# Kernel optimization log

Hardware: AMD Instinct MI355X
Metric: run time of the kernel (lower is better)

## Reference

```python
import jax, jax.numpy as jnp
import numpy as np

N = 100000        # nodes
E = 1600000       # edges (N * avg_degree 16)
D_IN = 128
D_OUT = 32
OBS_T = 60        # observation_time -> decay table size 60*OBS_T = 3600
T_MAX = 60 * OBS_T


def setup_inputs() -> dict:
    key = jax.random.key(0)
    ks = jax.random.split(key, 8)
    inp = {
        "input": jax.random.normal(ks[0], (N, D_IN), dtype=jnp.float32),
        "W": jax.random.normal(ks[1], (D_IN, D_OUT), dtype=jnp.float32) * (np.sqrt(2.0) / np.sqrt(D_IN)),
        # decay weights are abs(normal(0, 0.02)) in the original; rand*0.04 is same scale
        "decay_weight1": jnp.abs(jax.random.normal(ks[2], (T_MAX, 1), dtype=jnp.float32) * 0.02),
        "decay_weight2": jnp.abs(jax.random.normal(ks[3], (T_MAX, 1), dtype=jnp.float32) * 0.02),
        "edge_row": jax.random.randint(ks[4], (E,), 0, N, dtype=jnp.int32),
        "edge_col": jax.random.randint(ks[5], (E,), 0, N, dtype=jnp.int32),
        # zero-based interval index; equals (adj_value - 1) of the original code
        "edge_time": jax.random.randint(ks[6], (E,), 0, T_MAX, dtype=jnp.int32),
        "arrive_time": jax.random.randint(ks[7], (N,), 0, T_MAX, dtype=jnp.int32),
        "observation_time": OBS_T,
    }
    return inp


def reference(input, W, decay_weight1, decay_weight2,
              edge_row, edge_col, edge_time, arrive_time, observation_time):
    n_nodes = input.shape[0]
    # h = relu(input @ W)  [N, D_OUT]
    h = jax.nn.relu(jnp.matmul(input, W))
    # one-hot(interval) @ decay_weight1 == embedding lookup  -> per-edge decay scalar
    decay = decay_weight1[edge_time, 0]                        # [E]
    # SpecialSpmm: out[i] = sum_{edges (i,j)} decay_e * h[j]  (gather-scale-scatter)
    msgs = decay[:, None] * h[edge_col]                        # [E, D_OUT]
    h_prime = jax.ops.segment_sum(msgs, edge_row, num_segments=n_nodes)
    # outlayer window decay: one-hot(60*T - arrive - 1) @ decay_weight2 == lookup
    win_idx = 60 * observation_time - arrive_time - 1          # [N] in [0, 60*T)
    h_prime = decay_weight2[win_idx, 0][:, None] * h_prime
    return h_prime
```

## Files before the change

### kernel.cpp

```cpp
#include <hip/hip_runtime.h>

#define N_NODES 100000
#define N_EDGES 1600000
#define D_IN    128
#define D_OUT   32
#define RPB     16
#define NB      (N_NODES / RPB)
#define CROWS   2048
#define NCB     49
#define FPC     (CROWS / RPB)
#define NSH     8
#define CAP_A   4500
#define DEPTH   48
#define CAPF    352
#define GRID_A  2048
#define EPB_A   ((N_EDGES + GRID_A - 1) / GRID_A)

typedef __attribute__((ext_vector_type(8))) short bf16x8;
typedef __attribute__((ext_vector_type(4))) float f32x4;

__device__ inline short f2bf(float f) {
    union { float f; unsigned u; } v; v.f = f;
    unsigned r = (v.u + 0x7FFFu + ((v.u >> 16) & 1u)) >> 16;
    return (short)r;
}
__device__ inline float bf2f(unsigned short b) {
    return __uint_as_float((unsigned)b << 16);
}

__global__ __launch_bounds__(256) void wconv_kernel(
    const float* __restrict__ W, short* __restrict__ WbT)
{
    const int i = blockIdx.x * 256 + threadIdx.x;
    if (i >= D_IN * D_OUT) return;
    const int k = i >> 5, c = i & 31;
    WbT[c * D_IN + k] = f2bf(W[i]);
}

__global__ __launch_bounds__(256) void gemm_mfma_kernel(
    const float* __restrict__ in, const short* __restrict__ WbT,
    unsigned short* __restrict__ h16)
{
    const int wave = threadIdx.x >> 6;
    const int lane = threadIdx.x & 63;
    const int r0   = blockIdx.x * 64 + wave * 16;
    const int c16  = lane & 15;
    const int quad = lane >> 4;

    int ra = r0 + c16;
    if (ra >= N_NODES) ra = N_NODES - 1;
    const float* arow = in + (size_t)ra * D_IN;

    f32x4 acc0 = {0.f, 0.f, 0.f, 0.f};
    f32x4 acc1 = {0.f, 0.f, 0.f, 0.f};

#pragma unroll
    for (int q = 0; q < 4; ++q) {
        const float* ap = arow + q * 32 + quad * 8;
        f32x4 a0 = *(const f32x4*)(ap);
        f32x4 a1 = *(const f32x4*)(ap + 4);
        bf16x8 af;
        af[0] = f2bf(a0.x); af[1] = f2bf(a0.y); af[2] = f2bf(a0.z); af[3] = f2bf(a0.w);
        af[4] = f2bf(a1.x); af[5] = f2bf(a1.y); af[6] = f2bf(a1.z); af[7] = f2bf(a1.w);
        bf16x8 b0 = *(const bf16x8*)(WbT + (c16)      * D_IN + q * 32 + quad * 8);
        bf16x8 b1 = *(const bf16x8*)(WbT + (c16 + 16) * D_IN + q * 32 + quad * 8);
        acc0 = __builtin_amdgcn_mfma_f32_16x16x32_bf16(af, b0, acc0, 0, 0, 0);
        acc1 = __builtin_amdgcn_mfma_f32_16x16x32_bf16(af, b1, acc1, 0, 0, 0);
    }

#pragma unroll
    for (int i = 0; i < 4; ++i) {
        const int rr = r0 + quad * 4 + i;
        if (rr < N_NODES) {
            h16[(size_t)rr * D_OUT + c16]      = (unsigned short)f2bf(fmaxf(acc0[i], 0.f));
            h16[(size_t)rr * D_OUT + c16 + 16] = (unsigned short)f2bf(fmaxf(acc1[i], 0.f));
        }
    }
}

__global__ __launch_bounds__(256) void phaseA_kernel(
    const int* __restrict__ erow, const int* __restrict__ ecol,
    const int* __restrict__ etime, const float* __restrict__ dw1,
    int* __restrict__ gcur,
    uint2* __restrict__ segA)
{
    __shared__ uint2 lbin[NCB][DEPTH];
    __shared__ int   lcnt[NCB];
    __shared__ int   gbase[NCB];

    const int tid   = threadIdx.x;
    const int blk   = blockIdx.x;
    const int shard = blk & (NSH - 1);
    const int wv    = tid >> 6;
    const int ln    = tid & 63;

    if (tid < NCB) lcnt[tid] = 0;
    __syncthreads();

    const int e_beg = blk * EPB_A;
    const int e_end = min(e_beg + EPB_A, N_EDGES);

    for (int e = e_beg + tid; e < e_end; e += 256) {
        const int row = erow[e];
        const int cb  = row >> 11;
        uint2 p;
        p.x = (unsigned)ecol[e] | ((unsigned)(row & (CROWS - 1)) << 17);
        p.y = __float_as_uint(dw1[etime[e]]);
        const int pos = atomicAdd(&lcnt[cb], 1);
        if (pos < DEPTH) lbin[cb][pos] = p;
    }
    __syncthreads();

    if (tid < NCB) {
        const int c = min(lcnt[tid], DEPTH);
        gbase[tid] = atomicAdd(&gcur[(tid * NSH + shard) * 16], c);
    }
    __syncthreads();

    for (int bin = wv; bin < NCB; bin += 4) {
        const int c  = min(lcnt[bin], DEPTH);
        const int gb = gbase[bin];
        uint2* seg = segA + (size_t)(bin * NSH + shard) * CAP_A;
        for (int k = ln; k < c; k += 64) {
            if (gb + k < CAP_A) seg[gb + k] = lbin[bin][k];
        }
    }
}

__global__ __launch_bounds__(256) void phaseB_kernel(
    const int* __restrict__ gcur, const uint2* __restrict__ segA,
    int* __restrict__ fcur,
    uint2* __restrict__ spk2)
{
    __shared__ int hist[FPC];
    __shared__ int curs[FPC];

    const int tid   = threadIdx.x;
    const int cb    = blockIdx.x >> 3;
    const int shard = blockIdx.x & 7;
    const int n     = min(gcur[(cb * NSH + shard) * 16], CAP_A);
    const uint2* seg = segA + (size_t)(cb * NSH + shard) * CAP_A;

    if (tid < FPC) hist[tid] = 0;
    __syncthreads();

    for (int i = tid; i < n; i += 256)
        atomicAdd(&hist[(seg[i].x >> 21) & 127], 1);
    __syncthreads();

    if (tid < FPC) {
        const int h  = hist[tid];
        const int fb = cb * FPC + tid;
        curs[tid] = (h && fb < NB) ? atomicAdd(&fcur[fb], h) : 0;
    }
    __syncthreads();

    for (int i = tid; i < n; i += 256) {
        const uint2 p  = seg[i];
        const int   fl = (p.x >> 21) & 127;
        const int  pos = atomicAdd(&curs[fl], 1);
        if (pos < CAPF)
            spk2[(size_t)(cb * FPC + fl) * CAPF + pos] = p;
    }
}

__global__ __launch_bounds__(256) void bucket_reduce_kernel(
    const unsigned short* __restrict__ h16, const int* __restrict__ fcur,
    const uint2* __restrict__ spk2, const float* __restrict__ dw2,
    const int* __restrict__ arrive, const int* __restrict__ obs,
    float* __restrict__ out)
{
    __shared__ uint2 pk[CAPF];
    __shared__ uint2 pk2[CAPF];
    __shared__ int   bin[RPB];
    __shared__ int   start[RPB + 1];
    __shared__ int   cur[RPB];

    const int tid = threadIdx.x;
    const int b   = blockIdx.x;
    const int n   = min(fcur[b], CAPF);
    const uint2* seg = spk2 + (size_t)b * CAPF;

    if (tid < RPB) bin[tid] = 0;
    __syncthreads();

    for (int i = tid; i < n; i += 256) {
        const uint2 p = seg[i];
        pk[i] = p;
        atomicAdd(&bin[(p.x >> 17) & 15], 1);
    }
    __syncthreads();

    if (tid == 0) {
        int a = 0;
#pragma unroll
        for (int r = 0; r < RPB; ++r) { start[r] = a; cur[r] = a; a += bin[r]; }
        start[RPB] = a;
    }
    __syncthreads();

    for (int i = tid; i < n; i += 256) {
        const uint2 p = pk[i];
        pk2[atomicAdd(&cur[(p.x >> 17) & 15], 1)] = p;
    }
    __syncthreads();

    const int c = tid & 31;
    const int g = tid >> 5;
    const int T = 60 * obs[0];

#pragma unroll
    for (int rr = 0; rr < 2; ++rr) {
        const int rl  = g * 2 + rr;
        const int beg = start[rl];
        const int end = start[rl + 1];

        float acc = 0.f;
        int j = beg;
        for (; j + 4 <= end; j += 4) {
            const uint2 p0 = pk2[j];
            const uint2 p1 = pk2[j + 1];
            const uint2 p2 = pk2[j + 2];
            const uint2 p3 = pk2[j + 3];
            const float v0 = bf2f(h16[(size_t)(p0.x & 0x1FFFF) * D_OUT + c]);
            const float v1 = bf2f(h16[(size_t)(p1.x & 0x1FFFF) * D_OUT + c]);
            const float v2 = bf2f(h16[(size_t)(p2.x & 0x1FFFF) * D_OUT + c]);
            const float v3 = bf2f(h16[(size_t)(p3.x & 0x1FFFF) * D_OUT + c]);
            acc = fmaf(__uint_as_float(p0.y), v0, acc);
            acc = fmaf(__uint_as_float(p1.y), v1, acc);
            acc = fmaf(__uint_as_float(p2.y), v2, acc);
            acc = fmaf(__uint_as_float(p3.y), v3, acc);
        }
        for (; j < end; ++j) {
            const uint2 p = pk2[j];
            acc = fmaf(__uint_as_float(p.y),
                       bf2f(h16[(size_t)(p.x & 0x1FFFF) * D_OUT + c]), acc);
        }

        const int r = b * RPB + rl;
        const float sdw = dw2[T - arrive[r] - 1];
        out[(size_t)r * D_OUT + c] = acc * sdw;
    }
}

extern "C" void kernel_launch(void* const* d_in, const int* in_sizes, int n_in,
                              void* d_out, int out_size, void* d_ws, size_t ws_size,
                              hipStream_t stream)
{
    const float* input  = (const float*)d_in[0];
    const float* W      = (const float*)d_in[1];
    const float* dw1    = (const float*)d_in[2];
    const float* dw2    = (const float*)d_in[3];
    const int*   erow   = (const int*)d_in[4];
    const int*   ecol   = (const int*)d_in[5];
    const int*   etime  = (const int*)d_in[6];
    const int*   arrive = (const int*)d_in[7];
    const int*   obs    = (const int*)d_in[8];

    float* out = (float*)d_out;

    char* p = (char*)d_ws;
    unsigned short* h16 = (unsigned short*)p;
    p += (size_t)N_NODES * D_OUT * 2;
    p = (char*)(((size_t)p + 255) & ~(size_t)255);
    short* WbT = (short*)p;
    p += D_IN * D_OUT * 2;
    p = (char*)(((size_t)p + 255) & ~(size_t)255);
    int* gcur = (int*)p;
    p += (size_t)NCB * NSH * 16 * 4;
    int* fcur = (int*)p;
    p += (size_t)NB * 4;
    p = (char*)(((size_t)p + 255) & ~(size_t)255);
    uint2* segA = (uint2*)p;
    p += (size_t)NCB * NSH * CAP_A * 8;
    p = (char*)(((size_t)p + 255) & ~(size_t)255);
    uint2* spk2 = (uint2*)p;

    hipMemsetAsync(gcur, 0, (size_t)(NCB * NSH * 16 + NB) * 4, stream);

    wconv_kernel<<<(D_IN * D_OUT + 255) / 256, 256, 0, stream>>>(W, WbT);
    gemm_mfma_kernel<<<(N_NODES + 63) / 64, 256, 0, stream>>>(input, WbT, h16);
    phaseA_kernel<<<GRID_A, 256, 0, stream>>>(erow, ecol, etime, dw1, gcur, segA);
    phaseB_kernel<<<NCB * NSH, 256, 0, stream>>>(gcur, segA, fcur, spk2);
    bucket_reduce_kernel<<<NB, 256, 0, stream>>>(
        h16, fcur, spk2, dw2, arrive, obs, out);
}
```

Baseline: 185.9 us.

## Pack edge records into 32-bit words and defer decay lookup to reduce

Edge records in the final bucket array shrink from 8 bytes to a single 32-bit word: column (17 bits), local row (3 bits) and time index (12 bits). The decay-weight gather moves from phaseA into the reduce kernel, where the small 3600-entry table should stay cache-resident. Rows per bucket drop from 16 to 8 so each 32-thread group handles one row, with a smaller per-bucket capacity. phaseB is split across twice as many blocks, with a 256-bin histogram. The smaller buckets and tighter capacity (200 for about 128 expected edges) raise the risk of overflow silently dropping edges.

```diff
diff --git a/kernel.cpp b/kernel.cpp
--- a/kernel.cpp
+++ b/kernel.cpp
@@ -4,7 +4,7 @@
 #define N_EDGES 1600000
 #define D_IN    128
 #define D_OUT   32
-#define RPB     16
+#define RPB     8
 #define NB      (N_NODES / RPB)
 #define CROWS   2048
 #define NCB     49
@@ -12,7 +12,7 @@
 #define NSH     8
 #define CAP_A   4500
 #define DEPTH   48
-#define CAPF    352
+#define CAPF    200
 #define GRID_A  2048
 #define EPB_A   ((N_EDGES + GRID_A - 1) / GRID_A)
 
@@ -80,7 +80,7 @@
 
 __global__ __launch_bounds__(256) void phaseA_kernel(
     const int* __restrict__ erow, const int* __restrict__ ecol,
-    const int* __restrict__ etime, const float* __restrict__ dw1,
+    const int* __restrict__ etime,
     int* __restrict__ gcur,
     uint2* __restrict__ segA)
 {
@@ -105,7 +105,7 @@
         const int cb  = row >> 11;
         uint2 p;
         p.x = (unsigned)ecol[e] | ((unsigned)(row & (CROWS - 1)) << 17);
-        p.y = __float_as_uint(dw1[etime[e]]);
+        p.y = (unsigned)etime[e];
         const int pos = atomicAdd(&lcnt[cb], 1);
         if (pos < DEPTH) lbin[cb][pos] = p;
     }
@@ -130,64 +130,71 @@
 __global__ __launch_bounds__(256) void phaseB_kernel(
     const int* __restrict__ gcur, const uint2* __restrict__ segA,
     int* __restrict__ fcur,
-    uint2* __restrict__ spk2)
+    unsigned* __restrict__ spk2)
 {
     __shared__ int hist[FPC];
     __shared__ int curs[FPC];
 
-    const int tid   = threadIdx.x;
-    const int cb    = blockIdx.x >> 3;
-    const int shard = blockIdx.x & 7;
-    const int n     = min(gcur[(cb * NSH + shard) * 16], CAP_A);
+    const int tid    = threadIdx.x;
+    const int seg_id = blockIdx.x >> 1;
+    const int half   = blockIdx.x & 1;
+    const int cb     = seg_id >> 3;
+    const int shard  = seg_id & 7;
+    const int ntot   = min(gcur[(cb * NSH + shard) * 16], CAP_A);
+    const int nh     = (ntot + 1) >> 1;
+    const int beg    = half * nh;
+    const int end    = min(ntot, beg + nh);
     const uint2* seg = segA + (size_t)(cb * NSH + shard) * CAP_A;
 
-    if (tid < FPC) hist[tid] = 0;
-    __syncthreads();
-
-    for (int i = tid; i < n; i += 256)
-        atomicAdd(&hist[(seg[i].x >> 21) & 127], 1);
-    __syncthreads();
-
-    if (tid < FPC) {
+    hist[tid] = 0;
+    __syncthreads();
+
+    for (int i = beg + tid; i < end; i += 256)
+        atomicAdd(&hist[(seg[i].x >> 20) & 255], 1);
+    __syncthreads();
+
+    {
         const int h  = hist[tid];
         const int fb = cb * FPC + tid;
         curs[tid] = (h && fb < NB) ? atomicAdd(&fcur[fb], h) : 0;
     }
     __syncthreads();
 
-    for (int i = tid; i < n; i += 256) {
-        const uint2 p  = seg[i];
-        const int   fl = (p.x >> 21) & 127;
-        const int  pos = atomicAdd(&curs[fl], 1);
+    for (int i = beg + tid; i < end; i += 256) {
+        const uint2 p   = seg[i];
+        const unsigned crl = (p.x >> 17) & 2047u;
+        const int      fl  = crl >> 3;
+        const unsigned rec = (p.x & 0x1FFFFu) | ((crl & 7u) << 17) | (p.y << 20);
+        const int pos = atomicAdd(&curs[fl], 1);
         if (pos < CAPF)
-            spk2[(size_t)(cb * FPC + fl) * CAPF + pos] = p;
+            spk2[(size_t)(cb * FPC + fl) * CAPF + pos] = rec;
     }
 }
 
 __global__ __launch_bounds__(256) void bucket_reduce_kernel(
     const unsigned short* __restrict__ h16, const int* __restrict__ fcur,
-    const uint2* __restrict__ spk2, const float* __restrict__ dw2,
-    const int* __restrict__ arrive, const int* __restrict__ obs,
-    float* __restrict__ out)
-{
-    __shared__ uint2 pk[CAPF];
-    __shared__ uint2 pk2[CAPF];
-    __shared__ int   bin[RPB];
-    __shared__ int   start[RPB + 1];
-    __shared__ int   cur[RPB];
+    const unsigned* __restrict__ spk2, const float* __restrict__ dw1,
+    const float* __restrict__ dw2, const int* __restrict__ arrive,
+    const int* __restrict__ obs, float* __restrict__ out)
+{
+    __shared__ unsigned pk[CAPF];
+    __shared__ unsigned pks[CAPF];
+    __shared__ int bin[RPB];
+    __shared__ int start[RPB + 1];
+    __shared__ int cur[RPB];
 
     const int tid = threadIdx.x;
     const int b   = blockIdx.x;
     const int n   = min(fcur[b], CAPF);
-    const uint2* seg = spk2 + (size_t)b * CAPF;
+    const unsigned* seg = spk2 + (size_t)b * CAPF;
 
     if (tid < RPB) bin[tid] = 0;
     __syncthreads();
 
     for (int i = tid; i < n; i += 256) {
-        const uint2 p = seg[i];
+        const unsigned p = seg[i];
         pk[i] = p;
-        atomicAdd(&bin[(p.x >> 17) & 15], 1);
+        atomicAdd(&bin[(p >> 17) & 7], 1);
     }
     __syncthreads();
 
@@ -200,8 +207,8 @@
     __syncthreads();
 
     for (int i = tid; i < n; i += 256) {
-        const uint2 p = pk[i];
-        pk2[atomicAdd(&cur[(p.x >> 17) & 15], 1)] = p;
+        const unsigned p = pk[i];
+        pks[atomicAdd(&cur[(p >> 17) & 7], 1)] = p;
     }
     __syncthreads();
 
@@ -209,38 +216,38 @@
     const int g = tid >> 5;
     const int T = 60 * obs[0];
 
-#pragma unroll
-    for (int rr = 0; rr < 2; ++rr) {
-        const int rl  = g * 2 + rr;
-        const int beg = start[rl];
-        const int end = start[rl + 1];
-
-        float acc = 0.f;
-        int j = beg;
-        for (; j + 4 <= end; j += 4) {
-            const uint2 p0 = pk2[j];
-            const uint2 p1 = pk2[j + 1];
-            const uint2 p2 = pk2[j + 2];
-            const uint2 p3 = pk2[j + 3];
-            const float v0 = bf2f(h16[(size_t)(p0.x & 0x1FFFF) * D_OUT + c]);
-            const float v1 = bf2f(h16[(size_t)(p1.x & 0x1FFFF) * D_OUT + c]);
-            const float v2 = bf2f(h16[(size_t)(p2.x & 0x1FFFF) * D_OUT + c]);
-            const float v3 = bf2f(h16[(size_t)(p3.x & 0x1FFFF) * D_OUT + c]);
-            acc = fmaf(__uint_as_float(p0.y), v0, acc);
-            acc = fmaf(__uint_as_float(p1.y), v1, acc);
-            acc = fmaf(__uint_as_float(p2.y), v2, acc);
-            acc = fmaf(__uint_as_float(p3.y), v3, acc);
-        }
-        for (; j < end; ++j) {
-            const uint2 p = pk2[j];
-            acc = fmaf(__uint_as_float(p.y),
-                       bf2f(h16[(size_t)(p.x & 0x1FFFF) * D_OUT + c]), acc);
-        }
-
-        const int r = b * RPB + rl;
-        const float sdw = dw2[T - arrive[r] - 1];
-        out[(size_t)r * D_OUT + c] = acc * sdw;
-    }
+    const int beg = start[g];
+    const int end = start[g + 1];
+
+    float acc = 0.f;
+    int j = beg;
+    for (; j + 4 <= end; j += 4) {
+        const unsigned p0 = pks[j];
+        const unsigned p1 = pks[j + 1];
+        const unsigned p2 = pks[j + 2];
+        const unsigned p3 = pks[j + 3];
+        const float v0 = bf2f(h16[(size_t)(p0 & 0x1FFFF) * D_OUT + c]);
+        const float v1 = bf2f(h16[(size_t)(p1 & 0x1FFFF) * D_OUT + c]);
+        const float v2 = bf2f(h16[(size_t)(p2 & 0x1FFFF) * D_OUT + c]);
+        const float v3 = bf2f(h16[(size_t)(p3 & 0x1FFFF) * D_OUT + c]);
+        const float w0 = dw1[p0 >> 20];
+        const float w1 = dw1[p1 >> 20];
+        const float w2 = dw1[p2 >> 20];
+        const float w3 = dw1[p3 >> 20];
+        acc = fmaf(w0, v0, acc);
+        acc = fmaf(w1, v1, acc);
+        acc = fmaf(w2, v2, acc);
+        acc = fmaf(w3, v3, acc);
+    }
+    for (; j < end; ++j) {
+        const unsigned p = pks[j];
+        acc = fmaf(dw1[p >> 20],
+                   bf2f(h16[(size_t)(p & 0x1FFFF) * D_OUT + c]), acc);
+    }
+
+    const int r = b * RPB + g;
+    const float sdw = dw2[T - arrive[r] - 1];
+    out[(size_t)r * D_OUT + c] = acc * sdw;
 }
 
 extern "C" void kernel_launch(void* const* d_in, const int* in_sizes, int n_in,
@@ -274,14 +281,14 @@
     uint2* segA = (uint2*)p;
     p += (size_t)NCB * NSH * CAP_A * 8;
     p = (char*)(((size_t)p + 255) & ~(size_t)255);
-    uint2* spk2 = (uint2*)p;
+    unsigned* spk2 = (unsigned*)p;
 
     hipMemsetAsync(gcur, 0, (size_t)(NCB * NSH * 16 + NB) * 4, stream);
 
     wconv_kernel<<<(D_IN * D_OUT + 255) / 256, 256, 0, stream>>>(W, WbT);
     gemm_mfma_kernel<<<(N_NODES + 63) / 64, 256, 0, stream>>>(input, WbT, h16);
-    phaseA_kernel<<<GRID_A, 256, 0, stream>>>(erow, ecol, etime, dw1, gcur, segA);
-    phaseB_kernel<<<NCB * NSH, 256, 0, stream>>>(gcur, segA, fcur, spk2);
+    phaseA_kernel<<<GRID_A, 256, 0, stream>>>(erow, ecol, etime, gcur, segA);
+    phaseB_kernel<<<NCB * NSH * 2, 256, 0, stream>>>(gcur, segA, fcur, spk2);
     bucket_reduce_kernel<<<NB, 256, 0, stream>>>(
-        h16, fcur, spk2, dw2, arrive, obs, out);
-}
+        h16, fcur, spk2, dw1, dw2, arrive, obs, out);
+}
```

After: 184.7 us. About the same (-0.6%).
